# Performance work log

Hardware: AMD Instinct MI355X
Metric: run time of the kernel (lower is better)

## Reference

```python
import jax, jax.numpy as jnp
import numpy as np

# dims
B, S, H = 2, 256, 1024          # batch, global seq, global hidden
BH, NH = 384, 8                  # byte_hidden, num heads
HD = BH // NH                    # head dim = 48
P = 4                            # num_global_proj (seed byte positions)
S_C = 12                         # byte decode steps (= target.shape[2])
L = 4                            # num_byte_decoder_layers
V = 258                          # byte vocab (256 bytes + pad 256 + eos 257)
T = P + S_C
EOS = 257
SCALE = 1.0 / np.sqrt(HD)


def setup_inputs() -> dict:
    key = jax.random.key(0)
    ks = jax.random.split(key, 12)
    w = lambda k, shp: jax.random.normal(k, shp, jnp.float32) * 0.02
    return {
        "x": jax.random.normal(ks[0], (B, S, H), jnp.float32),
        "target": jax.random.randint(ks[1], (B, S, S_C), 0, V),
        "Wproj": w(ks[2], (H, P * BH)),
        "attn_norm": jnp.ones((L, BH), jnp.float32),
        "Wq": w(ks[3], (L, BH, BH)),
        "Wk": w(ks[4], (L, BH, BH)),
        "Wv": w(ks[5], (L, BH, BH)),
        "Wo": w(ks[6], (L, BH, BH)),
        "ffn_norm": jnp.ones((L, BH), jnp.float32),
        "W1": w(ks[7], (L, BH, 4 * BH)),
        "W2": w(ks[8], (L, 4 * BH, BH)),
        "Wlm": w(ks[9], (BH, V)),
    }


def _rms(x, g):
    return x * jax.lax.rsqrt(jnp.mean(x * x, -1, keepdims=True) + 1e-5) * g


def _block(x, kc, vc, pos, an, Wq, Wk, Wv, Wo, fn, W1, W2, causal):
    # x: [N, Lq, BH]; kc/vc: [N, T, NH, HD] KV caches; pos: static write offset
    N, Lq, _ = x.shape
    h = _rms(x, an)
    q = (h @ Wq).reshape(N, Lq, NH, HD)
    k = (h @ Wk).reshape(N, Lq, NH, HD)
    v = (h @ Wv).reshape(N, Lq, NH, HD)
    kc = jax.lax.dynamic_update_slice(kc, k, (0, pos, 0, 0))
    vc = jax.lax.dynamic_update_slice(vc, v, (0, pos, 0, 0))
    nk = pos + Lq
    sc = jnp.einsum('nqhd,nkhd->nhqk', q, kc[:, :nk]) * SCALE
    if causal:
        mask = jnp.arange(nk)[None, :] <= (pos + jnp.arange(Lq))[:, None]
        sc = jnp.where(mask[None, None], sc, jnp.float32(-1e30))
    p = jax.nn.softmax(sc, axis=-1)
    o = jnp.einsum('nhqk,nkhd->nqhd', p, vc[:, :nk]).reshape(N, Lq, BH)
    x = x + o @ Wo
    x = x + jax.nn.gelu(_rms(x, fn) @ W1, approximate=False) @ W2
    return x, kc, vc


def _forward(x, Wproj, attn_norm, Wq, Wk, Wv, Wo, ffn_norm, W1, W2, Wlm):
    N = B * S
    x0 = (x.reshape(N, H) @ Wproj).reshape(N, P, BH)
    x_out = jnp.zeros((N, T, BH), x0.dtype).at[:, :P].set(x0)
    kc = [jnp.zeros((N, T, NH, HD), x0.dtype) for _ in range(L)]
    vc = [jnp.zeros((N, T, NH, HD), x0.dtype) for _ in range(L)]
    finished = jnp.zeros((N,), bool)
    for i in range(S_C):
        if i == 0:
            pos, xi, causal = 0, x_out[:, :P], True          # prefill seed bytes
        else:
            pos, xi, causal = P + i - 1, x_out[:, P + i - 1:P + i], False  # decode 1 token
        for l in range(L):
            xi, kc[l], vc[l] = _block(xi, kc[l], vc[l], pos,
                                      attn_norm[l], Wq[l], Wk[l], Wv[l], Wo[l],
                                      ffn_norm[l], W1[l], W2[l], causal)
        gen = xi[:, -1]                                       # [N, BH]
        unf = ~finished
        # scatter only unfinished streams back (finished stay zero, as in torch)
        x_out = x_out.at[:, P + i].set(jnp.where(unf[:, None], gen, jnp.float32(0.0)))
        finished = finished | (unf & (jnp.argmax(gen, -1) == EOS))
    return x_out.reshape(B, S, T, BH)[:, :, P:, :] @ Wlm      # [B,S,S_C,V]


def reference(x, target, Wproj, attn_norm, Wq, Wk, Wv, Wo, ffn_norm, W1, W2, Wlm):
    del target  # only sets S_c (static here)
    return _forward(x, Wproj, attn_norm, Wq, Wk, Wv, Wo, ffn_norm, W1, W2, Wlm)
```

## Files before the change

kernel.cpp:

```cpp
#include <hip/hip_runtime.h>
#include <hip/hip_bf16.h>


constexpr int H_IN  = 1024;
constexpr int BH    = 384;
constexpr int NH    = 8;
constexpr int HD    = 48;
constexpr int PP    = 4;
constexpr int S_CNT = 12;
constexpr int NL    = 4;
constexpr int NV    = 258;
constexpr int TT    = 16;
constexpr int NSEQ  = 512;
constexpr int EOS_I = 257;
constexpr int NTH   = 768;
constexpr float RSCALE = 0.14433756729740646f;

typedef _Float16 h2 __attribute__((ext_vector_type(2)));
typedef _Float16 h8 __attribute__((ext_vector_type(8)));

union W16 { h8 v8; h2 h[4]; _Float16 e[8]; };

template<int N> struct IC { static constexpr int value = N; };

__device__ __forceinline__ float fdot2(h2 a, h2 b, float c) {
#if __has_builtin(__builtin_amdgcn_fdot2)
  return __builtin_amdgcn_fdot2(a, b, c, false);
#else
  return c + (float)a.x * (float)b.x + (float)a.y * (float)b.y;
#endif
}

template<typename T>
__device__ __forceinline__ T ntload(const T* p) { return __builtin_nontemporal_load(p); }
template<typename T>
__device__ __forceinline__ void ntstore(T* p, T v) { __builtin_nontemporal_store(v, p); }

__global__ __launch_bounds__(256)
void pack8_kernel(const float* __restrict__ src, const float* __restrict__ g,
                  h8* __restrict__ dst, int C) {
  int c  = blockIdx.x * 256 + threadIdx.x;
  int j8 = blockIdx.y;
  if (c < C) {
    h8 v;
    #pragma unroll
    for (int r = 0; r < 8; r++) {
      int row = 8 * j8 + r;
      float s = g ? g[row] : 1.0f;
      v[r] = (_Float16)(src[(size_t)row * C + c] * s);
    }
    dst[(size_t)j8 * C + c] = v;
  }
}

__global__ __launch_bounds__(NTH)
void decoder_kernel(const float* __restrict__ x,
                    const h8* __restrict__ Wproj8,
                    const h8* __restrict__ Wq8,
                    const h8* __restrict__ Wk8,
                    const h8* __restrict__ Wv8,
                    const h8* __restrict__ Wo8,
                    const h8* __restrict__ W18,
                    const h8* __restrict__ W28,
                    const h8* __restrict__ Wlm8,
                    float* __restrict__ out,
                    _Float16* __restrict__ kbuf,
                    _Float16* __restrict__ vbuf)
{
  __shared__ float xs[2][4][BH];
  __shared__ __align__(16) _Float16 xh[2][4][BH];
  __shared__ __align__(16) _Float16 qh[2][4][BH];
  __shared__ __align__(16) _Float16 oh[2][4][BH];
  __shared__ float sc[2][NH][4][TT];
  __shared__ __align__(16) union Scr {
    float qkvp[3][2][4][BH];
    float wop[2][4][BH];
    struct { __align__(16) _Float16 f1h[2][4][4*BH];
             float w2p[2][4][BH]; } ffn;
    __align__(16) _Float16 xin[2][H_IN];
  } scr;
  __shared__ float redsq[2][4][6];
  __shared__ float redv[12];
  __shared__ int   redi[12];
  __shared__ int   fin[2];

  const int tid = threadIdx.x;
  const int kg  = tid / BH;
  const int col = tid - kg * BH;
  const int sq  = kg;
  const int og  = 1 - kg;
  const int wid = tid >> 6;
  const int w6  = wid % 6;
  const int seq0 = blockIdx.x * 2;

  if (tid < 2) fin[tid] = 0;

  for (int s = 0; s < 2; s++) {
    const size_t base = (size_t)(seq0 + s) * H_IN;
    for (int j = tid; j < H_IN; j += NTH) scr.xin[s][j] = (_Float16)ntload(&x[base + j]);
  }
  __syncthreads();
  {
    float acc[2][2] = {};
    for (int j8 = 0; j8 < H_IN / 8; j8 += 4) {
      W16 w0[4], w1[4];
      #pragma unroll
      for (int u = 0; u < 4; u++) {
        w0[u].v8 = ntload(&Wproj8[(size_t)(j8 + u) * (PP * BH) + tid]);
        w1[u].v8 = ntload(&Wproj8[(size_t)(j8 + u) * (PP * BH) + tid + NTH]);
      }
      #pragma unroll
      for (int u = 0; u < 4; u++)
        #pragma unroll
        for (int s = 0; s < 2; s++) {
          W16 hv; hv.v8 = *(const h8*)&scr.xin[s][(j8 + u) * 8];
          #pragma unroll
          for (int r = 0; r < 4; r++) {
            acc[s][0] = fdot2(hv.h[r], w0[u].h[r], acc[s][0]);
            acc[s][1] = fdot2(hv.h[r], w1[u].h[r], acc[s][1]);
          }
        }
    }
    const int m0 = tid / BH, cc = tid - m0 * BH;
    #pragma unroll
    for (int s = 0; s < 2; s++) {
      xs[s][m0][cc]     = acc[s][0];  xh[s][m0][cc]     = (_Float16)acc[s][0];
      xs[s][m0 + 2][cc] = acc[s][1];  xh[s][m0 + 2][cc] = (_Float16)acc[s][1];
      float r0 = acc[s][0] * acc[s][0], r1 = acc[s][1] * acc[s][1];
      #pragma unroll
      for (int off = 32; off; off >>= 1) {
        r0 += __shfl_down(r0, off, 64); r1 += __shfl_down(r1, off, 64);
      }
      if ((tid & 63) == 0) { redsq[s][m0][w6] = r0; redsq[s][m0 + 2][w6] = r1; }
    }
  }
  __syncthreads();

  auto layers = [&](auto ntc, int pos, bool causal) {
    constexpr int NT = decltype(ntc)::value;
    const int nk = pos + NT;
    for (int l = 0; l < NL; l++) {
      {
        const size_t wb = ((size_t)l * 48 + kg * 24) * BH + col;
        float aq[2][NT] = {}, ak[2][NT] = {}, av[2][NT] = {};
        for (int j8 = 0; j8 < 24; j8 += 4) {
          W16 wq[4], wk[4], wv[4];
          #pragma unroll
          for (int u = 0; u < 4; u++) {
            wq[u].v8 = Wq8[wb + (size_t)(j8 + u) * BH];
            wk[u].v8 = Wk8[wb + (size_t)(j8 + u) * BH];
            wv[u].v8 = Wv8[wb + (size_t)(j8 + u) * BH];
          }
          #pragma unroll
          for (int u = 0; u < 4; u++)
            #pragma unroll
            for (int s = 0; s < 2; s++)
              #pragma unroll
              for (int tok = 0; tok < NT; tok++) {
                W16 hv; hv.v8 = *(const h8*)&xh[s][tok][(kg * 24 + j8 + u) * 8];
                #pragma unroll
                for (int r = 0; r < 4; r++) {
                  aq[s][tok] = fdot2(hv.h[r], wq[u].h[r], aq[s][tok]);
                  ak[s][tok] = fdot2(hv.h[r], wk[u].h[r], ak[s][tok]);
                  av[s][tok] = fdot2(hv.h[r], wv[u].h[r], av[s][tok]);
                }
              }
        }
        #pragma unroll
        for (int tok = 0; tok < NT; tok++) {
          scr.qkvp[0][og][tok][col] = aq[og][tok];
          scr.qkvp[1][og][tok][col] = ak[og][tok];
          scr.qkvp[2][og][tok][col] = av[og][tok];
        }
        __syncthreads();
        {
          const size_t cb = (((size_t)(seq0 + kg) * NL + l) * TT + pos) * BH + col;
          #pragma unroll
          for (int tok = 0; tok < NT; tok++) {
            float ss = redsq[kg][tok][0] + redsq[kg][tok][1] + redsq[kg][tok][2] +
                       redsq[kg][tok][3] + redsq[kg][tok][4] + redsq[kg][tok][5];
            float sca = rsqrtf(ss * (1.0f / BH) + 1e-5f);
            qh[kg][tok][col] = (_Float16)((aq[kg][tok] + scr.qkvp[0][kg][tok][col]) * sca * RSCALE);
            ntstore(&kbuf[cb + (size_t)tok * BH],
                    (_Float16)((ak[kg][tok] + scr.qkvp[1][kg][tok][col]) * sca));
            ntstore(&vbuf[cb + (size_t)tok * BH],
                    (_Float16)((av[kg][tok] + scr.qkvp[2][kg][tok][col]) * sca));
          }
        }
        __syncthreads();
      }
      {
        const int nu = 2 * NH * NT * nk;
        if (tid < nu) {
          int s = tid / (NH * NT * nk), r = tid % (NH * NT * nk);
          int h = r / (NT * nk); int r2 = r % (NT * nk);
          int qi = r2 / nk, j = r2 % nk;
          float d;
          if (causal && j > pos + qi) d = -1e30f;
          else {
            const h8* kp8 = (const h8*)(kbuf + (((size_t)(seq0 + s) * NL + l) * TT + j) * BH + h * HD);
            W16 kk[6];
            #pragma unroll
            for (int c = 0; c < 6; c++) kk[c].v8 = ntload(&kp8[c]);
            d = 0.f;
            #pragma unroll
            for (int c = 0; c < 6; c++)
              #pragma unroll
              for (int e = 0; e < 8; e++)
                d += (float)qh[s][qi][h * HD + c * 8 + e] * (float)kk[c].e[e];
          }
          sc[s][h][qi][j] = d;
        }
      }
      __syncthreads();
      {
        const int nr = 2 * NH * NT;
        if (tid < nr) {
          int s = tid / (NH * NT), r = tid % (NH * NT);
          int h = r / NT, qi = r % NT;
          float m = -3.0e38f;
          for (int j = 0; j < nk; j++) m = fmaxf(m, sc[s][h][qi][j]);
          float den = 0.f;
          for (int j = 0; j < nk; j++) {
            float e = expf(sc[s][h][qi][j] - m);
            sc[s][h][qi][j] = e; den += e;
          }
          float inv = 1.0f / den;
          for (int j = 0; j < nk; j++) sc[s][h][qi][j] *= inv;
        }
      }
      __syncthreads();
      {
        const size_t vb = (((size_t)(seq0 + sq) * NL + l) * TT) * BH + col;
        const int h = col / HD;
        #pragma unroll
        for (int tok = 0; tok < NT; tok++) {
          float acc = 0.f;
          int j = 0;
          for (; j + 4 <= nk; j += 4) {
            float v0 = (float)ntload(&vbuf[vb + (size_t)(j + 0) * BH]);
            float v1 = (float)ntload(&vbuf[vb + (size_t)(j + 1) * BH]);
            float v2 = (float)ntload(&vbuf[vb + (size_t)(j + 2) * BH]);
            float v3 = (float)ntload(&vbuf[vb + (size_t)(j + 3) * BH]);
            acc += sc[sq][h][tok][j] * v0 + sc[sq][h][tok][j+1] * v1 +
                   sc[sq][h][tok][j+2] * v2 + sc[sq][h][tok][j+3] * v3;
          }
          for (; j < nk; j++)
            acc += sc[sq][h][tok][j] * (float)ntload(&vbuf[vb + (size_t)j * BH]);
          oh[sq][tok][col] = (_Float16)acc;
        }
      }
      __syncthreads();
      {
        const size_t wb = ((size_t)l * 48 + kg * 24) * BH + col;
        float ao[2][NT] = {};
        for (int j8 = 0; j8 < 24; j8 += 8) {
          W16 w[8];
          #pragma unroll
          for (int u = 0; u < 8; u++) w[u].v8 = Wo8[wb + (size_t)(j8 + u) * BH];
          #pragma unroll
          for (int u = 0; u < 8; u++)
            #pragma unroll
            for (int s = 0; s < 2; s++)
              #pragma unroll
              for (int tok = 0; tok < NT; tok++) {
                W16 hv; hv.v8 = *(const h8*)&oh[s][tok][(kg * 24 + j8 + u) * 8];
                #pragma unroll
                for (int r = 0; r < 4; r++)
                  ao[s][tok] = fdot2(hv.h[r], w[u].h[r], ao[s][tok]);
              }
        }
        #pragma unroll
        for (int tok = 0; tok < NT; tok++) scr.wop[og][tok][col] = ao[og][tok];
        __syncthreads();
        #pragma unroll
        for (int tok = 0; tok < NT; tok++) {
          float xn = xs[kg][tok][col] + ao[kg][tok] + scr.wop[kg][tok][col];
          xs[kg][tok][col] = xn; xh[kg][tok][col] = (_Float16)xn;
          float r = xn * xn;
          #pragma unroll
          for (int off = 32; off; off >>= 1) r += __shfl_down(r, off, 64);
          if ((tid & 63) == 0) redsq[kg][tok][w6] = r;
        }
        __syncthreads();
      }
      {
        float a1[2][NT][2] = {};
        for (int j8 = 0; j8 < 48; j8 += 4) {
          W16 w0[4], w1[4];
          #pragma unroll
          for (int u = 0; u < 4; u++) {
            w0[u].v8 = W18[((size_t)(l * 48 + j8 + u)) * (4 * BH) + tid];
            w1[u].v8 = W18[((size_t)(l * 48 + j8 + u)) * (4 * BH) + tid + NTH];
          }
          #pragma unroll
          for (int u = 0; u < 4; u++)
            #pragma unroll
            for (int s = 0; s < 2; s++)
              #pragma unroll
              for (int t = 0; t < NT; t++) {
                W16 hv; hv.v8 = *(const h8*)&xh[s][t][(j8 + u) * 8];
                #pragma unroll
                for (int r = 0; r < 4; r++) {
                  a1[s][t][0] = fdot2(hv.h[r], w0[u].h[r], a1[s][t][0]);
                  a1[s][t][1] = fdot2(hv.h[r], w1[u].h[r], a1[s][t][1]);
                }
              }
        }
        #pragma unroll
        for (int s = 0; s < 2; s++)
          #pragma unroll
          for (int t = 0; t < NT; t++) {
            float ss = redsq[s][t][0] + redsq[s][t][1] + redsq[s][t][2] +
                       redsq[s][t][3] + redsq[s][t][4] + redsq[s][t][5];
            float sca = rsqrtf(ss * (1.0f / BH) + 1e-5f);
            float z0 = a1[s][t][0] * sca, z1 = a1[s][t][1] * sca;
            scr.ffn.f1h[s][t][tid]       = (_Float16)(0.5f * z0 * (1.0f + erff(z0 * 0.7071067811865476f)));
            scr.ffn.f1h[s][t][tid + NTH] = (_Float16)(0.5f * z1 * (1.0f + erff(z1 * 0.7071067811865476f)));
          }
        __syncthreads();
        {
          float a2[2][NT] = {};
          for (int j8 = 0; j8 < 96; j8 += 8) {
            W16 w[8];
            #pragma unroll
            for (int u = 0; u < 8; u++)
              w[u].v8 = W28[((size_t)(l * 192 + kg * 96 + j8 + u)) * BH + col];
            #pragma unroll
            for (int u = 0; u < 8; u++)
              #pragma unroll
              for (int s = 0; s < 2; s++)
                #pragma unroll
                for (int t = 0; t < NT; t++) {
                  W16 fv; fv.v8 = *(const h8*)&scr.ffn.f1h[s][t][(kg * 96 + j8 + u) * 8];
                  #pragma unroll
                  for (int r = 0; r < 4; r++)
                    a2[s][t] = fdot2(fv.h[r], w[u].h[r], a2[s][t]);
                }
          }
          #pragma unroll
          for (int t = 0; t < NT; t++) scr.ffn.w2p[og][t][col] = a2[og][t];
          __syncthreads();
          #pragma unroll
          for (int t = 0; t < NT; t++) {
            float xn = xs[kg][t][col] + a2[kg][t] + scr.ffn.w2p[kg][t][col];
            xs[kg][t][col] = xn; xh[kg][t][col] = (_Float16)xn;
            float r = xn * xn;
            #pragma unroll
            for (int off = 32; off; off >>= 1) r += __shfl_down(r, off, 64);
            if ((tid & 63) == 0) redsq[kg][t][w6] = r;
          }
          __syncthreads();
        }
      }
    }
  };

  for (int i = 0; i < S_CNT; i++) {
    int grow;
    if (i == 0) { layers(IC<4>{}, 0, true);           grow = 3; }
    else        { layers(IC<1>{}, PP + i - 1, false); grow = 0; }

    {
      float gen = xs[sq][grow][col];
      float v = gen; int idx = col;
      #pragma unroll
      for (int off = 32; off; off >>= 1) {
        float v2 = __shfl_down(v, off, 64); int i2 = __shfl_down(idx, off, 64);
        if (v2 > v || (v2 == v && i2 < idx)) { v = v2; idx = i2; }
      }
      if ((tid & 63) == 0) { redv[wid] = v; redi[wid] = idx; }
      float nxt = fin[sq] ? 0.0f : gen;
      xs[sq][0][col] = nxt; xh[sq][0][col] = (_Float16)nxt;
      float r = nxt * nxt;
      #pragma unroll
      for (int off = 32; off; off >>= 1) r += __shfl_down(r, off, 64);
      if ((tid & 63) == 0) redsq[sq][0][w6] = r;
      __syncthreads();
    }
    {
      if (col == 0) {
        const int b = sq * 6;
        float bv = redv[b]; int bi = redi[b];
        for (int w = 1; w < 6; w++)
          if (redv[b + w] > bv || (redv[b + w] == bv && redi[b + w] < bi)) {
            bv = redv[b + w]; bi = redi[b + w];
          }
        if (bi == EOS_I) fin[sq] = 1;
      }
      if (col < NV) {
        float acc = 0.f;
        for (int j8 = 0; j8 < 48; j8 += 8) {
          W16 w[8];
          #pragma unroll
          for (int u = 0; u < 8; u++) w[u].v8 = Wlm8[(size_t)(j8 + u) * NV + col];
          #pragma unroll
          for (int u = 0; u < 8; u++) {
            W16 gv; gv.v8 = *(const h8*)&xh[sq][0][(j8 + u) * 8];
            #pragma unroll
            for (int r = 0; r < 4; r++) acc = fdot2(gv.h[r], w[u].h[r], acc);
          }
        }
        ntstore(&out[((size_t)(seq0 + sq) * S_CNT + i) * NV + col], acc);
      }
      __syncthreads();
    }
  }
}

extern "C" void kernel_launch(void* const* d_in, const int* in_sizes, int n_in,
                              void* d_out, int out_size, void* d_ws, size_t ws_size,
                              hipStream_t stream) {
  const float* x     = (const float*)d_in[0];
  const float* Wproj = (const float*)d_in[2];
  const float* an    = (const float*)d_in[3];
  const float* Wq    = (const float*)d_in[4];
  const float* Wk    = (const float*)d_in[5];
  const float* Wv    = (const float*)d_in[6];
  const float* Wo    = (const float*)d_in[7];
  const float* fn    = (const float*)d_in[8];
  const float* W1    = (const float*)d_in[9];
  const float* W2    = (const float*)d_in[10];
  const float* Wlm   = (const float*)d_in[11];
  float* out = (float*)d_out;
  (void)ws_size; (void)in_sizes; (void)n_in; (void)out_size;

  h8* w = (h8*)d_ws;
  const int n_proj = (H_IN / 8) * (PP * BH);
  const int n_qkvo = NL * (BH / 8) * BH;
  const int n_w1   = NL * (BH / 8) * (4 * BH);
  const int n_w2   = NL * (4 * BH / 8) * BH;
  const int n_lm   = (BH / 8) * NV;
  h8* Wproj_p = w;  w += n_proj;
  h8* Wq_p    = w;  w += n_qkvo;
  h8* Wk_p    = w;  w += n_qkvo;
  h8* Wv_p    = w;  w += n_qkvo;
  h8* Wo_p    = w;  w += n_qkvo;
  h8* W1_p    = w;  w += n_w1;
  h8* W2_p    = w;  w += n_w2;
  h8* Wlm_p   = w;  w += n_lm;
  const size_t kv_elems = (size_t)NSEQ * NL * TT * BH;
  _Float16* kbuf = (_Float16*)w;
  _Float16* vbuf = kbuf + kv_elems;

  auto pack = [&](const float* src, const float* g, h8* dst, int R, int C) {
    dim3 grid((C + 255) / 256, R / 8);
    pack8_kernel<<<grid, 256, 0, stream>>>(src, g, dst, C);
  };
  pack(Wproj, nullptr, Wproj_p, H_IN,        PP * BH);
  pack(Wq,    an,      Wq_p,    NL * BH,     BH);
  pack(Wk,    an,      Wk_p,    NL * BH,     BH);
  pack(Wv,    an,      Wv_p,    NL * BH,     BH);
  pack(Wo,    nullptr, Wo_p,    NL * BH,     BH);
  pack(W1,    fn,      W1_p,    NL * BH,     4 * BH);
  pack(W2,    nullptr, W2_p,    NL * 4 * BH, BH);
  pack(Wlm,   nullptr, Wlm_p,   BH,          NV);

  decoder_kernel<<<NSEQ / 2, NTH, 0, stream>>>(
      x, Wproj_p, Wq_p, Wk_p, Wv_p, Wo_p, W1_p, W2_p, Wlm_p, out, kbuf, vbuf);
}
```

Measured before the change: 2.485 ms.

## Quantize FFN weights to uint8 with per-column scales and fp16 unpack

Packs W1 and W2 into offset-128 uint8 with per-output-column scales, which halves weight bytes per FFN step. In the kernel the bytes are unpacked to fp16 with the 0x6400 magic-number trick, and the offset is corrected using extra warp reductions of the activation sums. Nontemporal loads and stores are also switched back to regular accesses. The cost is lower weight precision, which may exceed tolerance, plus extra reductions and unpack instructions in the inner loop.

```diff
diff --git a/kernel.cpp b/kernel.cpp
--- a/kernel.cpp
+++ b/kernel.cpp
@@ -31,10 +31,20 @@
 #endif
 }
 
-template<typename T>
-__device__ __forceinline__ T ntload(const T* p) { return __builtin_nontemporal_load(p); }
-template<typename T>
-__device__ __forceinline__ void ntstore(T* p, T v) { __builtin_nontemporal_store(v, p); }
+__device__ __forceinline__ void unpack8(uint2 w, h2* o) {
+  union U { unsigned u; h2 h; } c;
+#if __has_builtin(__builtin_amdgcn_perm)
+  c.u = __builtin_amdgcn_perm(0x64646464u, w.x, 0x04010400u); o[0] = c.h;
+  c.u = __builtin_amdgcn_perm(0x64646464u, w.x, 0x04030402u); o[1] = c.h;
+  c.u = __builtin_amdgcn_perm(0x64646464u, w.y, 0x04010400u); o[2] = c.h;
+  c.u = __builtin_amdgcn_perm(0x64646464u, w.y, 0x04030402u); o[3] = c.h;
+#else
+  c.u = 0x64006400u | (w.x & 0xffu) | ((w.x & 0xff00u) << 8);            o[0] = c.h;
+  c.u = 0x64006400u | ((w.x >> 16) & 0xffu) | ((w.x >> 8) & 0xff0000u);  o[1] = c.h;
+  c.u = 0x64006400u | (w.y & 0xffu) | ((w.y & 0xff00u) << 8);            o[2] = c.h;
+  c.u = 0x64006400u | ((w.y >> 16) & 0xffu) | ((w.y >> 8) & 0xff0000u);  o[3] = c.h;
+#endif
+}
 
 __global__ __launch_bounds__(256)
 void pack8_kernel(const float* __restrict__ src, const float* __restrict__ g,
@@ -53,6 +63,45 @@
   }
 }
 
+__global__ __launch_bounds__(256)
+void scaleq_kernel(const float* __restrict__ src, const float* __restrict__ g,
+                   float* __restrict__ sc, int R, int C) {
+  int c = blockIdx.x * 256 + threadIdx.x;
+  int l = blockIdx.y;
+  if (c < C) {
+    float m = 0.f;
+    for (int k = 0; k < R; k++) {
+      float gv = g ? g[l * R + k] : 1.f;
+      m = fmaxf(m, fabsf(src[((size_t)l * R + k) * C + c] * gv));
+    }
+    sc[l * C + c] = (m > 0.f) ? (m / 127.f) : 1.f;
+  }
+}
+
+__global__ __launch_bounds__(256)
+void packq_kernel(const float* __restrict__ src, const float* __restrict__ g,
+                  const float* __restrict__ sc, uint2* __restrict__ dst, int R, int C) {
+  int c  = blockIdx.x * 256 + threadIdx.x;
+  int j8 = blockIdx.y;
+  if (c < C) {
+    int row0 = 8 * j8;
+    int l = row0 / R;
+    float s = sc[l * C + c];
+    unsigned lo = 0, hi = 0;
+    #pragma unroll
+    for (int r = 0; r < 8; r++) {
+      int row = row0 + r, rl = row - l * R;
+      float gv = g ? g[l * R + rl] : 1.f;
+      float w = src[(size_t)row * C + c] * gv;
+      int q = (int)rintf(w / s) + 128;
+      q = q < 0 ? 0 : (q > 255 ? 255 : q);
+      if (r < 4) lo |= ((unsigned)q) << (8 * r);
+      else       hi |= ((unsigned)q) << (8 * (r - 4));
+    }
+    dst[(size_t)j8 * C + c] = make_uint2(lo, hi);
+  }
+}
+
 __global__ __launch_bounds__(NTH)
 void decoder_kernel(const float* __restrict__ x,
                     const h8* __restrict__ Wproj8,
@@ -60,8 +109,10 @@
                     const h8* __restrict__ Wk8,
                     const h8* __restrict__ Wv8,
                     const h8* __restrict__ Wo8,
-                    const h8* __restrict__ W18,
-                    const h8* __restrict__ W28,
+                    const uint2* __restrict__ W1q,
+                    const uint2* __restrict__ W2q,
+                    const float* __restrict__ s1,
+                    const float* __restrict__ s2,
                     const h8* __restrict__ Wlm8,
                     float* __restrict__ out,
                     _Float16* __restrict__ kbuf,
@@ -80,6 +131,8 @@
     __align__(16) _Float16 xin[2][H_IN];
   } scr;
   __shared__ float redsq[2][4][6];
+  __shared__ float redA [2][4][6];
+  __shared__ float redA2[2][4][2][12];
   __shared__ float redv[12];
   __shared__ int   redi[12];
   __shared__ int   fin[2];
@@ -97,7 +150,7 @@
 
   for (int s = 0; s < 2; s++) {
     const size_t base = (size_t)(seq0 + s) * H_IN;
-    for (int j = tid; j < H_IN; j += NTH) scr.xin[s][j] = (_Float16)ntload(&x[base + j]);
+    for (int j = tid; j < H_IN; j += NTH) scr.xin[s][j] = (_Float16)x[base + j];
   }
   __syncthreads();
   {
@@ -106,8 +159,8 @@
       W16 w0[4], w1[4];
       #pragma unroll
       for (int u = 0; u < 4; u++) {
-        w0[u].v8 = ntload(&Wproj8[(size_t)(j8 + u) * (PP * BH) + tid]);
-        w1[u].v8 = ntload(&Wproj8[(size_t)(j8 + u) * (PP * BH) + tid + NTH]);
+        w0[u].v8 = Wproj8[(size_t)(j8 + u) * (PP * BH) + tid];
+        w1[u].v8 = Wproj8[(size_t)(j8 + u) * (PP * BH) + tid + NTH];
       }
       #pragma unroll
       for (int u = 0; u < 4; u++)
@@ -181,10 +234,8 @@
                        redsq[kg][tok][3] + redsq[kg][tok][4] + redsq[kg][tok][5];
             float sca = rsqrtf(ss * (1.0f / BH) + 1e-5f);
             qh[kg][tok][col] = (_Float16)((aq[kg][tok] + scr.qkvp[0][kg][tok][col]) * sca * RSCALE);
-            ntstore(&kbuf[cb + (size_t)tok * BH],
-                    (_Float16)((ak[kg][tok] + scr.qkvp[1][kg][tok][col]) * sca));
-            ntstore(&vbuf[cb + (size_t)tok * BH],
-                    (_Float16)((av[kg][tok] + scr.qkvp[2][kg][tok][col]) * sca));
+            kbuf[cb + (size_t)tok * BH] = (_Float16)((ak[kg][tok] + scr.qkvp[1][kg][tok][col]) * sca);
+            vbuf[cb + (size_t)tok * BH] = (_Float16)((av[kg][tok] + scr.qkvp[2][kg][tok][col]) * sca);
           }
         }
         __syncthreads();
@@ -201,7 +252,7 @@
             const h8* kp8 = (const h8*)(kbuf + (((size_t)(seq0 + s) * NL + l) * TT + j) * BH + h * HD);
             W16 kk[6];
             #pragma unroll
-            for (int c = 0; c < 6; c++) kk[c].v8 = ntload(&kp8[c]);
+            for (int c = 0; c < 6; c++) kk[c].v8 = kp8[c];
             d = 0.f;
             #pragma unroll
             for (int c = 0; c < 6; c++)
@@ -238,15 +289,15 @@
           float acc = 0.f;
           int j = 0;
           for (; j + 4 <= nk; j += 4) {
-            float v0 = (float)ntload(&vbuf[vb + (size_t)(j + 0) * BH]);
-            float v1 = (float)ntload(&vbuf[vb + (size_t)(j + 1) * BH]);
-            float v2 = (float)ntload(&vbuf[vb + (size_t)(j + 2) * BH]);
-            float v3 = (float)ntload(&vbuf[vb + (size_t)(j + 3) * BH]);
+            float v0 = (float)vbuf[vb + (size_t)(j + 0) * BH];
+            float v1 = (float)vbuf[vb + (size_t)(j + 1) * BH];
+            float v2 = (float)vbuf[vb + (size_t)(j + 2) * BH];
+            float v3 = (float)vbuf[vb + (size_t)(j + 3) * BH];
             acc += sc[sq][h][tok][j] * v0 + sc[sq][h][tok][j+1] * v1 +
                    sc[sq][h][tok][j+2] * v2 + sc[sq][h][tok][j+3] * v3;
           }
           for (; j < nk; j++)
-            acc += sc[sq][h][tok][j] * (float)ntload(&vbuf[vb + (size_t)j * BH]);
+            acc += sc[sq][h][tok][j] * (float)vbuf[vb + (size_t)j * BH];
           oh[sq][tok][col] = (_Float16)acc;
         }
       }
@@ -276,25 +327,33 @@
         #pragma unroll
         for (int tok = 0; tok < NT; tok++) {
           float xn = xs[kg][tok][col] + ao[kg][tok] + scr.wop[kg][tok][col];
-          xs[kg][tok][col] = xn; xh[kg][tok][col] = (_Float16)xn;
+          _Float16 xh16 = (_Float16)xn;
+          xs[kg][tok][col] = xn; xh[kg][tok][col] = xh16;
           float r = xn * xn;
-          #pragma unroll
-          for (int off = 32; off; off >>= 1) r += __shfl_down(r, off, 64);
-          if ((tid & 63) == 0) redsq[kg][tok][w6] = r;
+          float a = (float)xh16;
+          #pragma unroll
+          for (int off = 32; off; off >>= 1) {
+            r += __shfl_down(r, off, 64); a += __shfl_down(a, off, 64);
+          }
+          if ((tid & 63) == 0) { redsq[kg][tok][w6] = r; redA[kg][tok][w6] = a; }
         }
         __syncthreads();
       }
       {
+        const float s1a = s1[l * (4 * BH) + tid];
+        const float s1b = s1[l * (4 * BH) + tid + NTH];
         float a1[2][NT][2] = {};
         for (int j8 = 0; j8 < 48; j8 += 4) {
-          W16 w0[4], w1[4];
+          uint2 wa[4], wb2[4];
           #pragma unroll
           for (int u = 0; u < 4; u++) {
-            w0[u].v8 = W18[((size_t)(l * 48 + j8 + u)) * (4 * BH) + tid];
-            w1[u].v8 = W18[((size_t)(l * 48 + j8 + u)) * (4 * BH) + tid + NTH];
-          }
-          #pragma unroll
-          for (int u = 0; u < 4; u++)
+            wa[u]  = W1q[((size_t)(l * 48 + j8 + u)) * (4 * BH) + tid];
+            wb2[u] = W1q[((size_t)(l * 48 + j8 + u)) * (4 * BH) + tid + NTH];
+          }
+          #pragma unroll
+          for (int u = 0; u < 4; u++) {
+            h2 w0[4], w1h[4];
+            unpack8(wa[u], w0); unpack8(wb2[u], w1h);
             #pragma unroll
             for (int s = 0; s < 2; s++)
               #pragma unroll
@@ -302,32 +361,47 @@
                 W16 hv; hv.v8 = *(const h8*)&xh[s][t][(j8 + u) * 8];
                 #pragma unroll
                 for (int r = 0; r < 4; r++) {
-                  a1[s][t][0] = fdot2(hv.h[r], w0[u].h[r], a1[s][t][0]);
-                  a1[s][t][1] = fdot2(hv.h[r], w1[u].h[r], a1[s][t][1]);
+                  a1[s][t][0] = fdot2(hv.h[r], w0[r],  a1[s][t][0]);
+                  a1[s][t][1] = fdot2(hv.h[r], w1h[r], a1[s][t][1]);
                 }
               }
+          }
         }
         #pragma unroll
         for (int s = 0; s < 2; s++)
           #pragma unroll
           for (int t = 0; t < NT; t++) {
+            float Af = redA[s][t][0] + redA[s][t][1] + redA[s][t][2] +
+                       redA[s][t][3] + redA[s][t][4] + redA[s][t][5];
             float ss = redsq[s][t][0] + redsq[s][t][1] + redsq[s][t][2] +
                        redsq[s][t][3] + redsq[s][t][4] + redsq[s][t][5];
             float sca = rsqrtf(ss * (1.0f / BH) + 1e-5f);
-            float z0 = a1[s][t][0] * sca, z1 = a1[s][t][1] * sca;
-            scr.ffn.f1h[s][t][tid]       = (_Float16)(0.5f * z0 * (1.0f + erff(z0 * 0.7071067811865476f)));
-            scr.ffn.f1h[s][t][tid + NTH] = (_Float16)(0.5f * z1 * (1.0f + erff(z1 * 0.7071067811865476f)));
+            float z0 = s1a * (a1[s][t][0] - 1152.f * Af) * sca;
+            float z1 = s1b * (a1[s][t][1] - 1152.f * Af) * sca;
+            _Float16 g0 = (_Float16)(0.5f * z0 * (1.0f + erff(z0 * 0.7071067811865476f)));
+            _Float16 g1 = (_Float16)(0.5f * z1 * (1.0f + erff(z1 * 0.7071067811865476f)));
+            scr.ffn.f1h[s][t][tid]       = g0;
+            scr.ffn.f1h[s][t][tid + NTH] = g1;
+            float a0f = (float)g0, a1f = (float)g1;
+            #pragma unroll
+            for (int off = 32; off; off >>= 1) {
+              a0f += __shfl_down(a0f, off, 64); a1f += __shfl_down(a1f, off, 64);
+            }
+            if ((tid & 63) == 0) { redA2[s][t][0][wid] = a0f; redA2[s][t][1][wid] = a1f; }
           }
         __syncthreads();
         {
+          const float s2c = s2[l * BH + col];
           float a2[2][NT] = {};
           for (int j8 = 0; j8 < 96; j8 += 8) {
-            W16 w[8];
+            uint2 w[8];
             #pragma unroll
             for (int u = 0; u < 8; u++)
-              w[u].v8 = W28[((size_t)(l * 192 + kg * 96 + j8 + u)) * BH + col];
-            #pragma unroll
-            for (int u = 0; u < 8; u++)
+              w[u] = W2q[((size_t)(l * 192 + kg * 96 + j8 + u)) * BH + col];
+            #pragma unroll
+            for (int u = 0; u < 8; u++) {
+              h2 wh[4];
+              unpack8(w[u], wh);
               #pragma unroll
               for (int s = 0; s < 2; s++)
                 #pragma unroll
@@ -335,15 +409,25 @@
                   W16 fv; fv.v8 = *(const h8*)&scr.ffn.f1h[s][t][(kg * 96 + j8 + u) * 8];
                   #pragma unroll
                   for (int r = 0; r < 4; r++)
-                    a2[s][t] = fdot2(fv.h[r], w[u].h[r], a2[s][t]);
+                    a2[s][t] = fdot2(fv.h[r], wh[r], a2[s][t]);
                 }
-          }
-          #pragma unroll
-          for (int t = 0; t < NT; t++) scr.ffn.w2p[og][t][col] = a2[og][t];
+            }
+          }
+          #pragma unroll
+          for (int t = 0; t < NT; t++) {
+            float A2o = 0.f;
+            #pragma unroll
+            for (int wq_ = 0; wq_ < 12; wq_++) A2o += redA2[og][t][kg][wq_];
+            scr.ffn.w2p[og][t][col] = s2c * (a2[og][t] - 1152.f * A2o);
+          }
           __syncthreads();
           #pragma unroll
           for (int t = 0; t < NT; t++) {
-            float xn = xs[kg][t][col] + a2[kg][t] + scr.ffn.w2p[kg][t][col];
+            float A2s = 0.f;
+            #pragma unroll
+            for (int wq_ = 0; wq_ < 12; wq_++) A2s += redA2[kg][t][kg][wq_];
+            float own = s2c * (a2[kg][t] - 1152.f * A2s);
+            float xn = xs[kg][t][col] + own + scr.ffn.w2p[kg][t][col];
             xs[kg][t][col] = xn; xh[kg][t][col] = (_Float16)xn;
             float r = xn * xn;
             #pragma unroll
@@ -401,7 +485,7 @@
             for (int r = 0; r < 4; r++) acc = fdot2(gv.h[r], w[u].h[r], acc);
           }
         }
-        ntstore(&out[((size_t)(seq0 + sq) * S_CNT + i) * NV + col], acc);
+        out[((size_t)(seq0 + sq) * S_CNT + i) * NV + col] = acc;
       }
       __syncthreads();
     }
@@ -425,37 +509,49 @@
   float* out = (float*)d_out;
   (void)ws_size; (void)in_sizes; (void)n_in; (void)out_size;
 
-  h8* w = (h8*)d_ws;
-  const int n_proj = (H_IN / 8) * (PP * BH);
-  const int n_qkvo = NL * (BH / 8) * BH;
-  const int n_w1   = NL * (BH / 8) * (4 * BH);
-  const int n_w2   = NL * (4 * BH / 8) * BH;
-  const int n_lm   = (BH / 8) * NV;
-  h8* Wproj_p = w;  w += n_proj;
-  h8* Wq_p    = w;  w += n_qkvo;
-  h8* Wk_p    = w;  w += n_qkvo;
-  h8* Wv_p    = w;  w += n_qkvo;
-  h8* Wo_p    = w;  w += n_qkvo;
-  h8* W1_p    = w;  w += n_w1;
-  h8* W2_p    = w;  w += n_w2;
-  h8* Wlm_p   = w;  w += n_lm;
+  char* p = (char*)d_ws;
+  const size_t n_proj = (H_IN / 8) * (PP * BH);
+  const size_t n_qkvo = NL * (BH / 8) * BH;
+  const size_t n_w1q  = (size_t)NL * (BH / 8) * (4*BH);
+  const size_t n_w2q  = (size_t)NL * (4*BH / 8) * BH;
+  const size_t n_lm   = (BH / 8) * NV;
+  h8* Wproj_p = (h8*)p;     p += n_proj * 16;
+  h8* Wq_p    = (h8*)p;     p += n_qkvo * 16;
+  h8* Wk_p    = (h8*)p;     p += n_qkvo * 16;
+  h8* Wv_p    = (h8*)p;     p += n_qkvo * 16;
+  h8* Wo_p    = (h8*)p;     p += n_qkvo * 16;
+  uint2* W1_q = (uint2*)p;  p += n_w1q * 8;
+  uint2* W2_q = (uint2*)p;  p += n_w2q * 8;
+  h8* Wlm_p   = (h8*)p;     p += n_lm * 16;
   const size_t kv_elems = (size_t)NSEQ * NL * TT * BH;
-  _Float16* kbuf = (_Float16*)w;
-  _Float16* vbuf = kbuf + kv_elems;
+  _Float16* kbuf = (_Float16*)p;  p += kv_elems * 2;
+  _Float16* vbuf = (_Float16*)p;  p += kv_elems * 2;
+  float* s1_p = (float*)p;  p += (size_t)NL * 4 * BH * 4;
+  float* s2_p = (float*)p;
 
   auto pack = [&](const float* src, const float* g, h8* dst, int R, int C) {
     dim3 grid((C + 255) / 256, R / 8);
     pack8_kernel<<<grid, 256, 0, stream>>>(src, g, dst, C);
   };
-  pack(Wproj, nullptr, Wproj_p, H_IN,        PP * BH);
-  pack(Wq,    an,      Wq_p,    NL * BH,     BH);
-  pack(Wk,    an,      Wk_p,    NL * BH,     BH);
-  pack(Wv,    an,      Wv_p,    NL * BH,     BH);
-  pack(Wo,    nullptr, Wo_p,    NL * BH,     BH);
-  pack(W1,    fn,      W1_p,    NL * BH,     4 * BH);
-  pack(W2,    nullptr, W2_p,    NL * 4 * BH, BH);
-  pack(Wlm,   nullptr, Wlm_p,   BH,          NV);
+  pack(Wproj, nullptr, Wproj_p, H_IN,    PP * BH);
+  pack(Wq,    an,      Wq_p,    NL * BH, BH);
+  pack(Wk,    an,      Wk_p,    NL * BH, BH);
+  pack(Wv,    an,      Wv_p,    NL * BH, BH);
+  pack(Wo,    nullptr, Wo_p,    NL * BH, BH);
+  pack(Wlm,   nullptr, Wlm_p,   BH,      NV);
+
+  {
+    dim3 g1((4 * BH + 255) / 256, NL);
+    scaleq_kernel<<<g1, 256, 0, stream>>>(W1, fn, s1_p, BH, 4 * BH);
+    dim3 g2((BH + 255) / 256, NL);
+    scaleq_kernel<<<g2, 256, 0, stream>>>(W2, nullptr, s2_p, 4 * BH, BH);
+    dim3 p1((4 * BH + 255) / 256, NL * BH / 8);
+    packq_kernel<<<p1, 256, 0, stream>>>(W1, fn, s1_p, W1_q, BH, 4 * BH);
+    dim3 p2((BH + 255) / 256, NL * 4 * BH / 8);
+    packq_kernel<<<p2, 256, 0, stream>>>(W2, nullptr, s2_p, W2_q, 4 * BH, BH);
+  }
 
   decoder_kernel<<<NSEQ / 2, NTH, 0, stream>>>(
-      x, Wproj_p, Wq_p, Wk_p, Wv_p, Wo_p, W1_p, W2_p, Wlm_p, out, kbuf, vbuf);
-}
+      x, Wproj_p, Wq_p, Wk_p, Wv_p, Wo_p, W1_q, W2_q, s1_p, s2_p, Wlm_p,
+      out, kbuf, vbuf);
+}
```

Result: slower. 3.071 ms (+23.6%).
